# Kernel tuning notes

Hardware: AMD Instinct MI355X
Metric: run time of the kernel (lower is better)

The kernel has to match this reference:

```python
import jax, jax.numpy as jnp
import numpy as np

DIM = 1024
HEADS = 16
HD = DIM // HEADS          # 64
HID = 4 * DIM              # 4096
TPF = 1374                 # tokens_per_frame
LR = 0.1
NS_ITERS = 5
TTT_STEPS = 2
B, S = 2, 4
SN = S * TPF               # 5496


def _newton_schulz(G, iters=NS_ITERS):
    """Muon Newton-Schulz orthogonalization (quintic iteration)."""
    a, b, c = 3.4445, -4.7750, 2.0315
    X = G / (jnp.linalg.norm(G) + 1e-7)
    transposed = G.shape[0] > G.shape[1]
    if transposed:
        X = X.T
    for _ in range(iters):
        A = X @ X.T                      # [m,m], m = min(rows, cols)
        X = a * X + (b * A + c * (A @ A)) @ X
    return X.T if transposed else X


def _muon_update(p, g):
    return p - LR * _newton_schulz(g)


def setup_inputs() -> dict:
    key = jax.random.key(0)
    ks = jax.random.split(key, 8)
    inp = {
        "x": jax.random.normal(ks[0], (B, SN, DIM), jnp.float32),
        "qkv_w": jax.random.normal(ks[1], (DIM, 3 * DIM), jnp.float32) * (DIM ** -0.5),
        "qkv_b": jnp.zeros((3 * DIM,), jnp.float32),
        "qn_scale": jnp.ones((HD,), jnp.float32),
        "qn_bias": jnp.zeros((HD,), jnp.float32),
        "kn_scale": jnp.ones((HD,), jnp.float32),
        "kn_bias": jnp.zeros((HD,), jnp.float32),
        # theta: lecun-normal scale (std = 1/sqrt(fan_in))
        "ttt_gate": jax.random.normal(ks[2], (DIM, HID), jnp.float32) * (DIM ** -0.5),
        "ttt_val": jax.random.normal(ks[3], (DIM, HID), jnp.float32) * (DIM ** -0.5),
        "ttt_proj": jax.random.normal(ks[4], (HID, DIM), jnp.float32) * (HID ** -0.5),
        "proj_w": jax.random.normal(ks[5], (DIM, DIM), jnp.float32) * (DIM ** -0.5),
        "proj_b": jnp.zeros((DIM,), jnp.float32),
    }
    return inp


def reference(x, qkv_w, qkv_b, qn_scale, qn_bias, kn_scale, kn_bias,
              ttt_gate, ttt_val, ttt_proj, proj_w, proj_b):
    Bx, SNx, _ = x.shape
    qkv = x @ qkv_w + qkv_b                       # [B, SN, 3*DIM]
    q, k, v = jnp.split(qkv, 3, axis=-1)
    q = q.reshape(Bx, SNx, HEADS, HD)
    k = k.reshape(Bx, SNx, HEADS, HD)
    # per-head L2 normalize then affine NormLayer (x*scale + bias)
    q = q / (jnp.linalg.norm(q, axis=-1, keepdims=True) + 1e-6) * qn_scale + qn_bias
    k = k / (jnp.linalg.norm(k, axis=-1, keepdims=True) + 1e-6) * kn_scale + kn_bias
    q_ttt = q.reshape(-1, DIM)                    # [B*SN, DIM]
    k_ttt = k.reshape(-1, DIM)
    # no short_conv param at init -> v_mixed is identity, so v_target == v
    v_ttt = v.reshape(-1, DIM)

    theta = {"gate": ttt_gate, "val": ttt_val, "proj": ttt_proj}

    def loss_fn(p):
        h = jax.nn.swish(k_ttt @ p["gate"]) * (k_ttt @ p["val"])   # [B*SN, HID]
        pred = h @ p["proj"]                                        # [B*SN, DIM]
        return jnp.mean((pred - v_ttt) ** 2)

    for _ in range(TTT_STEPS):
        grads = jax.grad(loss_fn)(theta)
        theta = {kk: _muon_update(theta[kk], grads[kk]) for kk in theta}

    h_q = jax.nn.swish(q_ttt @ theta["gate"]) * (q_ttt @ theta["val"])
    o = (h_q @ theta["proj"]) @ proj_w + proj_b
    return o.reshape(Bx, SNx, DIM)
```

## Files before the change

### kernel.cpp

```cpp
#include <hip/hip_runtime.h>
#include <stdint.h>

#define NTOK 10992
#define NTOKA 11264
#define FCHK 5632
#define PMi 4194304

typedef unsigned short u16;
typedef __attribute__((ext_vector_type(8))) __bf16 b8;
typedef __attribute__((ext_vector_type(4))) float f32x4;

__device__ __forceinline__ u16 f2b(float f) {
  union { float f; uint32_t u; } v; v.f = f;
  return (u16)((v.u + 0x7fffu + ((v.u >> 16) & 1u)) >> 16);
}
__device__ __forceinline__ float b2f(u16 b) {
  union { uint32_t u; float f; } v; v.u = ((uint32_t)b) << 16; return v.f;
}
__device__ __forceinline__ uint2 pk4(u16 a, u16 b, u16 c, u16 d) {
  uint2 r; r.x = (uint32_t)a | ((uint32_t)b << 16); r.y = (uint32_t)c | ((uint32_t)d << 16);
  return r;
}
__device__ __forceinline__ void gload16(const u16* g, u16* l) {
  __builtin_amdgcn_global_load_lds((const __attribute__((address_space(1))) void*)(const void*)g,
                                   (__attribute__((address_space(3))) void*)(void*)l, 16, 0, 0);
}

struct GA {
  const u16* A[3]; const u16* B[3];
  void* C[3]; u16* O1[3]; u16* OT[3];
  const void* E0[3]; const u16* E1[3];
  int lda[3], ldb[3];
  int M, N, K, ldc, ldo1, ldt, lde0, lde1;
  float p0, p1;
};

template <int EPI, int SPLIT>
__global__ __launch_bounds__(256, 2) void gemm_bt(GA g) {
  __shared__ u16 As[128 * 32];
  __shared__ u16 Bs[128 * 32];
  int bz = blockIdx.z, koff = 0, klen = g.K;
  if constexpr (SPLIT) { koff = (bz & 1) * (g.K >> 1); bz >>= 1; klen = g.K >> 1; }
  const u16* __restrict__ A = g.A[bz] + koff;
  const u16* __restrict__ B = g.B[bz] + koff;
  const int lda = g.lda[bz], ldb = g.ldb[bz];
  const int m0 = blockIdx.y * 128, n0 = blockIdx.x * 128;
  const int tid = threadIdx.x, w = tid >> 6, lane = tid & 63;
  const int wr = (w >> 1) * 64, wc = (w & 1) * 64;
  const int ln = lane & 15, lq = lane >> 4;

  f32x4 acc[4][4];
#pragma unroll
  for (int i = 0; i < 4; ++i)
#pragma unroll
    for (int j = 0; j < 4; ++j)
#pragma unroll
      for (int r = 0; r < 4; ++r) acc[i][j][r] = 0.f;

  const u16* Ag = A + (size_t)(m0 + 32 * w + (lane >> 2)) * lda + (lane & 3) * 8;
  const u16* Bg = B + (size_t)(n0 + 32 * w + (lane >> 2)) * ldb + (lane & 3) * 8;
  u16* AsW = &As[w * 1024];
  u16* BsW = &Bs[w * 1024];
  const int nkt = klen >> 5;

  for (int kt = 0; kt < nkt; ++kt) {
    __syncthreads();
    gload16(Ag, AsW);
    gload16(Ag + (size_t)16 * lda, AsW + 512);
    gload16(Bg, BsW);
    gload16(Bg + (size_t)16 * ldb, BsW + 512);
    Ag += 32; Bg += 32;
    __syncthreads();
    b8 af[4], bfr[4];
#pragma unroll
    for (int i = 0; i < 4; ++i) af[i] = *(const b8*)&As[(wr + i * 16 + ln) * 32 + lq * 8];
#pragma unroll
    for (int j = 0; j < 4; ++j) bfr[j] = *(const b8*)&Bs[(wc + j * 16 + ln) * 32 + lq * 8];
#pragma unroll
    for (int i = 0; i < 4; ++i)
#pragma unroll
      for (int j = 0; j < 4; ++j)
        acc[i][j] = __builtin_amdgcn_mfma_f32_16x16x32_bf16(af[i], bfr[j], acc[i][j], 0, 0, 0);
  }

  float* Cf = (float*)g.C[bz];
  u16* Cb = (u16*)g.C[bz];
  u16* O1 = g.O1[bz];
  u16* OT = g.OT[bz];
  const float* E0f = (const float*)g.E0[bz];
  const u16* E0b = (const u16*)g.E0[bz];
  const u16* E1b = g.E1[bz];

#pragma unroll
  for (int i = 0; i < 4; ++i) {
    const int mb = m0 + wr + i * 16 + lq * 4;
    if (mb >= g.M) continue;
#pragma unroll
    for (int j = 0; j < 4; ++j) {
      const int n = n0 + wc + j * 16 + ln;
      if (n >= g.N) continue;
      float vv[4];
#pragma unroll
      for (int r = 0; r < 4; ++r) vv[r] = acc[i][j][r];
      if constexpr (EPI == 0) {
#pragma unroll
        for (int r = 0; r < 4; ++r) Cb[(size_t)(mb + r) * g.ldc + n] = f2b(vv[r]);
      } else if constexpr (EPI == 1) {
        const float bias = E0f[n];
#pragma unroll
        for (int r = 0; r < 4; ++r) Cb[(size_t)(mb + r) * g.ldc + n] = f2b(vv[r] + bias);
      } else if constexpr (EPI == 3) {
        u16 oq[4];
#pragma unroll
        for (int r = 0; r < 4; ++r) {
          const int m = mb + r;
          Cb[(size_t)m * g.ldc + n] = f2b(vv[r]);
          const float zg = b2f(E0b[(size_t)m * g.lde0 + n]);
          const float s = 1.f / (1.f + __expf(-zg));
          const u16 ub = f2b(zg * s * vv[r]);
          O1[(size_t)m * g.ldo1 + n] = ub;
          oq[r] = ub;
        }
        *(uint2*)&OT[(size_t)n * g.ldt + mb] = pk4(oq[0], oq[1], oq[2], oq[3]);
      } else if constexpr (EPI == 4) {
#pragma unroll
        for (int r = 0; r < 4; ++r) {
          const int m = mb + r;
          const float zg = b2f(E0b[(size_t)m * g.lde0 + n]);
          const float s = 1.f / (1.f + __expf(-zg));
          Cb[(size_t)m * g.ldc + n] = f2b(zg * s * vv[r]);
        }
      } else if constexpr (EPI == 5) {
        u16 cq[4], oq[4];
#pragma unroll
        for (int r = 0; r < 4; ++r) {
          const int m = mb + r;
          const float zg = b2f(E0b[(size_t)m * g.lde0 + n]);
          const float zv = b2f(E1b[(size_t)m * g.lde1 + n]);
          const float s = 1.f / (1.f + __expf(-zg));
          cq[r] = f2b(vv[r] * zv * s * (1.f + zg * (1.f - s)));
          oq[r] = f2b(vv[r] * zg * s);
        }
        *(uint2*)&Cb[(size_t)n * g.ldt + mb] = pk4(cq[0], cq[1], cq[2], cq[3]);
        *(uint2*)&O1[(size_t)n * g.ldt + mb] = pk4(oq[0], oq[1], oq[2], oq[3]);
      } else if constexpr (EPI == 6) {
        const float bias = E0f[n];
#pragma unroll
        for (int r = 0; r < 4; ++r) Cf[(size_t)(mb + r) * g.ldc + n] = vv[r] + bias;
      } else if constexpr (EPI == 8) {
#pragma unroll
        for (int r = 0; r < 4; ++r) atomicAdd(&Cf[(size_t)(mb + r) * g.ldc + n], vv[r]);
      } else if constexpr (EPI == 9) {
        u16 cq[4];
#pragma unroll
        for (int r = 0; r < 4; ++r) {
          const int m = mb + r;
          const u16 ub = f2b(g.p0 * b2f(E0b[(size_t)m * g.lde0 + n]) + vv[r]);
          Cb[(size_t)m * g.ldc + n] = ub;
          cq[r] = ub;
        }
        *(uint2*)&OT[(size_t)n * g.ldt + mb] = pk4(cq[0], cq[1], cq[2], cq[3]);
      }
    }
  }
}

template <int EPI>
__global__ __launch_bounds__(256, 2) void gemm64(GA g) {
  __shared__ u16 As[64 * 32];
  __shared__ u16 Bs[64 * 32];
  const int bz = blockIdx.z;
  const u16* __restrict__ A = g.A[bz];
  const u16* __restrict__ B = g.B[bz];
  const int lda = g.lda[bz], ldb = g.ldb[bz];
  const int m0 = blockIdx.y * 64, n0 = blockIdx.x * 64;
  const int tid = threadIdx.x, w = tid >> 6, lane = tid & 63;
  const int wr = (w >> 1) * 32, wc = (w & 1) * 32;
  const int ln = lane & 15, lq = lane >> 4;

  f32x4 acc[2][2];
#pragma unroll
  for (int i = 0; i < 2; ++i)
#pragma unroll
    for (int j = 0; j < 2; ++j)
#pragma unroll
      for (int r = 0; r < 4; ++r) acc[i][j][r] = 0.f;

  const u16* Ag = A + (size_t)(m0 + 16 * w + (lane >> 2)) * lda + (lane & 3) * 8;
  const u16* Bg = B + (size_t)(n0 + 16 * w + (lane >> 2)) * ldb + (lane & 3) * 8;
  u16* AsW = &As[w * 512];
  u16* BsW = &Bs[w * 512];
  const int nkt = g.K >> 5;

  for (int kt = 0; kt < nkt; ++kt) {
    __syncthreads();
    gload16(Ag, AsW);
    gload16(Bg, BsW);
    Ag += 32; Bg += 32;
    __syncthreads();
    b8 af[2], bfr[2];
#pragma unroll
    for (int i = 0; i < 2; ++i) af[i] = *(const b8*)&As[(wr + i * 16 + ln) * 32 + lq * 8];
#pragma unroll
    for (int j = 0; j < 2; ++j) bfr[j] = *(const b8*)&Bs[(wc + j * 16 + ln) * 32 + lq * 8];
#pragma unroll
    for (int i = 0; i < 2; ++i)
#pragma unroll
      for (int j = 0; j < 2; ++j)
        acc[i][j] = __builtin_amdgcn_mfma_f32_16x16x32_bf16(af[i], bfr[j], acc[i][j], 0, 0, 0);
  }

  float* Cf = (float*)g.C[bz];
  u16* Cb = (u16*)g.C[bz];
  u16* OT = g.OT[bz];
  const float* E0f = (const float*)g.E0[bz];
  const u16* E0b = (const u16*)g.E0[bz];

#pragma unroll
  for (int i = 0; i < 2; ++i) {
    const int mb = m0 + wr + i * 16 + lq * 4;
    if (mb >= g.M) continue;
#pragma unroll
    for (int j = 0; j < 2; ++j) {
      const int n = n0 + wc + j * 16 + ln;
      if (n >= g.N) continue;
      float vv[4];
#pragma unroll
      for (int r = 0; r < 4; ++r) vv[r] = acc[i][j][r];
      if constexpr (EPI == 0) {
#pragma unroll
        for (int r = 0; r < 4; ++r) Cb[(size_t)(mb + r) * g.ldc + n] = f2b(vv[r]);
      } else if constexpr (EPI == 2) {
        u16 cq[4];
#pragma unroll
        for (int r = 0; r < 4; ++r) {
          const int m = mb + r;
          const u16 ub = f2b((vv[r] - b2f(E0b[(size_t)m * g.lde0 + n])) * g.p0);
          Cb[(size_t)m * g.ldc + n] = ub;
          cq[r] = ub;
        }
        *(uint2*)&OT[(size_t)n * g.ldt + mb] = pk4(cq[0], cq[1], cq[2], cq[3]);
      } else if constexpr (EPI == 6) {
        const float bias = E0f[n];
#pragma unroll
        for (int r = 0; r < 4; ++r) Cf[(size_t)(mb + r) * g.ldc + n] = vv[r] + bias;
      } else if constexpr (EPI == 7) {
#pragma unroll
        for (int r = 0; r < 4; ++r) {
          const int m = mb + r;
          Cb[(size_t)m * g.ldc + n] =
              f2b(g.p0 * b2f(E0b[(size_t)m * g.lde0 + n]) + g.p1 * vv[r]);
        }
      }
    }
  }
}

__global__ __launch_bounds__(256) void norm_qkv(const u16* __restrict__ qkvB,
    const float* __restrict__ qs, const float* __restrict__ qbi,
    const float* __restrict__ ks, const float* __restrict__ kbi,
    u16* __restrict__ qb, u16* __restrict__ kb, u16* __restrict__ vb) {
  const int tok = blockIdx.x;
  const int t = threadIdx.x;
  const int d = t * 4;
  const u16* row = qkvB + (size_t)tok * 3072;
  const uint2 qu = *(const uint2*)(row + d);
  const uint2 ku = *(const uint2*)(row + 1024 + d);
  *(uint2*)(vb + (size_t)tok * 1024 + d) = *(const uint2*)(row + 2048 + d);
  float q0 = b2f(qu.x & 0xffff), q1 = b2f(qu.x >> 16), q2 = b2f(qu.y & 0xffff), q3 = b2f(qu.y >> 16);
  float k0 = b2f(ku.x & 0xffff), k1 = b2f(ku.x >> 16), k2 = b2f(ku.y & 0xffff), k3 = b2f(ku.y >> 16);
  float sq = q0 * q0 + q1 * q1 + q2 * q2 + q3 * q3;
  float sk = k0 * k0 + k1 * k1 + k2 * k2 + k3 * k3;
  for (int off = 1; off < 16; off <<= 1) { sq += __shfl_xor(sq, off); sk += __shfl_xor(sk, off); }
  const float rq = 1.f / (sqrtf(sq) + 1e-6f);
  const float rk = 1.f / (sqrtf(sk) + 1e-6f);
  const int hd = d & 63;
  const float4 qsv = *(const float4*)(qs + hd);
  const float4 qbv = *(const float4*)(qbi + hd);
  const float4 ksv = *(const float4*)(ks + hd);
  const float4 kbv = *(const float4*)(kbi + hd);
  uint64_t pq = (uint64_t)f2b(q0 * rq * qsv.x + qbv.x)
              | ((uint64_t)f2b(q1 * rq * qsv.y + qbv.y) << 16)
              | ((uint64_t)f2b(q2 * rq * qsv.z + qbv.z) << 32)
              | ((uint64_t)f2b(q3 * rq * qsv.w + qbv.w) << 48);
  uint64_t pk = (uint64_t)f2b(k0 * rk * ksv.x + kbv.x)
              | ((uint64_t)f2b(k1 * rk * ksv.y + kbv.y) << 16)
              | ((uint64_t)f2b(k2 * rk * ksv.z + kbv.z) << 32)
              | ((uint64_t)f2b(k3 * rk * ksv.w + kbv.w) << 48);
  *(uint64_t*)(qb + (size_t)tok * 1024 + d) = pq;
  *(uint64_t*)(kb + (size_t)tok * 1024 + d) = pk;
}

__global__ __launch_bounds__(256) void tr_b16(const u16* __restrict__ in, u16* __restrict__ out,
                                              int Cin, int Rtot, int Rval,
                                              size_t inStr, size_t outStr) {
  const int b = blockIdx.z;
  in += (size_t)b * inStr; out += (size_t)b * outStr;
  __shared__ u16 t[32][33];
  const int c0 = blockIdx.x * 32, r0 = blockIdx.y * 32;
  const int tx = threadIdx.x, ty = threadIdx.y;
#pragma unroll
  for (int yy = 0; yy < 4; ++yy) {
    const int rr = ty * 4 + yy;
    const int r = r0 + rr;
    t[rr][tx] = (r < Rval) ? in[(size_t)r * Cin + c0 + tx] : (u16)0;
  }
  __syncthreads();
#pragma unroll
  for (int yy = 0; yy < 4; ++yy) {
    const int cc = ty * 4 + yy;
    out[(size_t)(c0 + cc) * Rtot + r0 + tx] = t[tx][cc];
  }
}

__global__ __launch_bounds__(256) void tr_f32b(const float* __restrict__ in, u16* __restrict__ out,
                                               int Cin, int Rtot) {
  __shared__ u16 t[32][33];
  const int c0 = blockIdx.x * 32, r0 = blockIdx.y * 32;
  const int tx = threadIdx.x, ty = threadIdx.y;
#pragma unroll
  for (int yy = 0; yy < 4; ++yy) {
    const int rr = ty * 4 + yy;
    t[rr][tx] = f2b(in[(size_t)(r0 + rr) * Cin + c0 + tx]);
  }
  __syncthreads();
#pragma unroll
  for (int yy = 0; yy < 4; ++yy) {
    const int cc = ty * 4 + yy;
    out[(size_t)(c0 + cc) * Rtot + r0 + tx] = t[tx][cc];
  }
}

__global__ void cvt_k(const float* __restrict__ in, u16* __restrict__ out, int n) {
  const int i = blockIdx.x * 256 + threadIdx.x;
  if (i < n) out[i] = f2b(in[i]);
}

__global__ void diag_k(float* __restrict__ out, int n, float val) {
  const int i = blockIdx.x * 256 + threadIdx.x;
  if (i < n) out[i] = val;
}

__global__ __launch_bounds__(256) void sumsq_k(const float* __restrict__ g, float* __restrict__ out) {
  const int b = blockIdx.y;
  const float* p = g + (size_t)b * PMi;
  float s = 0.f;
  for (int i = blockIdx.x * 256 + threadIdx.x; i < PMi; i += gridDim.x * 256) {
    float v = p[i]; s += v * v;
  }
  for (int off = 32; off > 0; off >>= 1) s += __shfl_xor(s, off);
  __shared__ float red[4];
  if ((threadIdx.x & 63) == 0) red[threadIdx.x >> 6] = s;
  __syncthreads();
  if (threadIdx.x == 0) atomicAdd(out + b, red[0] + red[1] + red[2] + red[3]);
}

__global__ __launch_bounds__(256) void scale_k(const float* __restrict__ g, const float* __restrict__ ss,
                                               u16* __restrict__ Xb) {
  const int b = blockIdx.y;
  const float r = 1.f / (sqrtf(ss[b]) + 1e-7f);
  const size_t o = (size_t)b * PMi;
  for (int i = blockIdx.x * 256 + threadIdx.x; i < PMi; i += gridDim.x * 256)
    Xb[o + i] = f2b(g[o + i] * r);
}

__global__ __launch_bounds__(256) void muon_apply(const u16* __restrict__ Xb_,
    u16* __restrict__ Gt, u16* __restrict__ Vt, u16* __restrict__ Pt, u16* __restrict__ Pb) {
  const int b = blockIdx.z;
  __shared__ float xs[32][33];
  __shared__ u16 ns[32][33];
  const int j0 = blockIdx.x * 32;
  const int i0 = blockIdx.y * 32;
  const u16* X = Xb_ + (size_t)b * PMi;
  const int tx = threadIdx.x, ty = threadIdx.y;
#pragma unroll
  for (int yy = 0; yy < 4; ++yy) {
    const int r = ty * 4 + yy;
    xs[r][tx] = b2f(X[(size_t)(i0 + r) * 4096 + j0 + tx]);
  }
  __syncthreads();
  if (b < 2) {
    u16* T = b ? Vt : Gt;
#pragma unroll
    for (int yy = 0; yy < 4; ++yy) {
      const int rr = ty * 4 + yy;
      const size_t idx = (size_t)(j0 + rr) * 1024 + i0 + tx;
      T[idx] = f2b(b2f(T[idx]) - 0.1f * xs[tx][rr]);
    }
  } else {
#pragma unroll
    for (int yy = 0; yy < 4; ++yy) {
      const int rr = ty * 4 + yy;
      const size_t idx = (size_t)(j0 + rr) * 1024 + i0 + tx;
      const float nv = b2f(Pb[idx]) - 0.1f * xs[tx][rr];
      const u16 nb = f2b(nv);
      Pb[idx] = nb;
      ns[rr][tx] = nb;
    }
    __syncthreads();
#pragma unroll
    for (int yy = 0; yy < 4; ++yy) {
      const int rr = ty * 4 + yy;
      Pt[(size_t)(i0 + rr) * 4096 + j0 + tx] = ns[tx][rr];
    }
  }
}

static GA mk(const u16* A, const u16* B, void* C, int M, int N, int K,
             int lda, int ldb, int ldc) {
  GA a{};
  a.A[0] = a.A[1] = a.A[2] = A;
  a.B[0] = a.B[1] = a.B[2] = B;
  a.C[0] = a.C[1] = a.C[2] = C;
  a.lda[0] = a.lda[1] = a.lda[2] = lda;
  a.ldb[0] = a.ldb[1] = a.ldb[2] = ldb;
  a.M = M; a.N = N; a.K = K; a.ldc = ldc;
  return a;
}

extern "C" void kernel_launch(void* const* d_in, const int* in_sizes, int n_in,
                              void* d_out, int out_size, void* d_ws, size_t ws_size,
                              hipStream_t stream) {
  (void)in_sizes; (void)n_in;
  const float* x      = (const float*)d_in[0];
  const float* qkv_w  = (const float*)d_in[1];
  const float* qkv_b  = (const float*)d_in[2];
  const float* qn_s   = (const float*)d_in[3];
  const float* qn_b   = (const float*)d_in[4];
  const float* kn_s   = (const float*)d_in[5];
  const float* kn_b   = (const float*)d_in[6];
  const float* g_gate = (const float*)d_in[7];
  const float* g_val  = (const float*)d_in[8];
  const float* g_proj = (const float*)d_in[9];
  const float* proj_w = (const float*)d_in[10];
  const float* proj_b = (const float*)d_in[11];
  float* out = (float*)d_out;

  const size_t PM = PMi;
  const size_t TD = (size_t)NTOKA * 1024;

  const size_t NEED1 = 253231360 + 4096;
  const size_t NEED2 = 127926528 + 177209344 + 4096;
  if (ws_size < NEED1) {
    diag_k<<<dim3((out_size + 255) / 256), dim3(256), 0, stream>>>(out, out_size,
                                                                   (float)(ws_size >> 20));
    return;
  }
  const int CHKr = (ws_size >= NEED2) ? 2816 : 1408;

  char* p = (char*)d_ws;
  auto carve = [&](size_t bytes) { char* r = p; p += (bytes + 255) & ~(size_t)255; return (void*)r; };
  auto cdiv = [](int a, int b) { return (a + b - 1) / b; };

  u16* Gt     = (u16*)carve(PM * 2);
  u16* Vt     = (u16*)carve(PM * 2);
  u16* Pt     = (u16*)carve(PM * 2);
  u16* Pb     = (u16*)carve(PM * 2);
  u16* projWt = (u16*)carve(1048576ull * 2);
  u16* qb     = (u16*)carve(TD * 2);
  u16* kb     = (u16*)carve(TD * 2);
  u16* vT     = (u16*)carve(TD * 2);
  u16* kT     = (u16*)carve(TD * 2);
  float* ssq  = (float*)carve(256);
  char* arena = p;

  u16* xb     = (u16*)arena;
  u16* qkvWt  = (u16*)(arena + 23068672);
  u16* qkvB   = (u16*)(arena + 29360128);
  u16* vb_tmp = (u16*)(arena + 96894976);
  const size_t CB = (size_t)CHKr * 4096 * 2;
  const size_t DP = (size_t)CHKr * 1024 * 2;
  u16* zg     = (u16*)arena;
  u16* zv     = (u16*)(arena + CB);
  u16* hh     = (u16*)(arena + 2 * CB);
  u16* hT     = (u16*)(arena + 3 * CB);
  u16* dzvT   = (u16*)(arena + 4 * CB);
  u16* dpredT = (u16*)(arena + 5 * CB);
  u16* dpredb = (u16*)(arena + 5 * CB + DP);
  float* gAll = (float*)(arena + 5 * CB + 2 * DP);
  u16* XAb  = (u16*)arena;
  u16* XAbT = (u16*)(arena + 25165824);
  u16* XBb  = (u16*)(arena + 50331648);
  u16* XBbT = (u16*)(arena + 75497472);
  u16* Ab   = (u16*)(arena + 100663296);
  u16* Wb   = (u16*)(arena + 106954752);
  u16* zgc = (u16*)arena;
  u16* oc  = (u16*)(arena + 46137344);

  const dim3 blk(256), tb32(32, 8);
  const float inv2 = 2.0f / (10992.0f * 1024.0f);
  const float nsa = 3.4445f, nsb = -4.7750f, nsc = 2.0315f;

  cvt_k<<<dim3(43968), blk, 0, stream>>>(x, xb, NTOK * 1024);
  cvt_k<<<dim3(16384), blk, 0, stream>>>(g_proj, Pb, (int)PM);
  tr_f32b<<<dim3(96, 32), tb32, 0, stream>>>(qkv_w, qkvWt, 3072, 1024);
  tr_f32b<<<dim3(32, 32), tb32, 0, stream>>>(proj_w, projWt, 1024, 1024);
  tr_f32b<<<dim3(128, 32), tb32, 0, stream>>>(g_gate, Gt, 4096, 1024);
  tr_f32b<<<dim3(128, 32), tb32, 0, stream>>>(g_val, Vt, 4096, 1024);
  tr_f32b<<<dim3(32, 128), tb32, 0, stream>>>(g_proj, Pt, 1024, 4096);

  {
    GA a = mk(xb, qkvWt, qkvB, NTOK, 3072, 1024, 1024, 1024, 3072);
    a.E0[0] = a.E0[1] = a.E0[2] = qkv_b;
    gemm_bt<1, 0><<<dim3(24, 86, 1), blk, 0, stream>>>(a);
  }
  norm_qkv<<<dim3(NTOK), blk, 0, stream>>>(qkvB, qn_s, qn_b, kn_s, kn_b, qb, kb, vb_tmp);
  tr_b16<<<dim3(32, 352, 1), tb32, 0, stream>>>(kb, kT, 1024, NTOKA, NTOK, 0, 0);
  tr_b16<<<dim3(32, 352, 1), tb32, 0, stream>>>(vb_tmp, vT, 1024, NTOKA, NTOK, 0, 0);

  for (int step = 0; step < 2; ++step) {
    hipMemsetAsync(gAll, 0, 3 * PM * 4, stream);
    for (int c0 = 0; c0 < NTOK; c0 += CHKr) {
      const int vc = (NTOK - c0 < CHKr) ? (NTOK - c0) : CHKr;
      const int mt = cdiv(vc, 128);
      const u16* kc = kb + (size_t)c0 * 1024;
      if (vc < CHKr)
        hipMemsetAsync(hT, 0, 2 * CB + DP, stream);
      gemm_bt<0, 0><<<dim3(32, mt, 1), blk, 0, stream>>>(
          mk(kc, Gt, zg, vc, 4096, 1024, 1024, 1024, 4096));
      {
        GA a = mk(kc, Vt, zv, vc, 4096, 1024, 1024, 1024, 4096);
        a.O1[0] = hh; a.ldo1 = 4096; a.OT[0] = hT; a.ldt = CHKr;
        a.E0[0] = zg; a.lde0 = 4096;
        gemm_bt<3, 0><<<dim3(32, mt, 1), blk, 0, stream>>>(a);
      }
      {
        GA a = mk(Pt, hh, dpredT, 1024, vc, 4096, 4096, 4096, CHKr);
        a.OT[0] = dpredb; a.ldt = 1024;
        a.E0[0] = vT + c0; a.lde0 = NTOKA; a.p0 = inv2;
        gemm64<2><<<dim3(cdiv(vc, 64), 16, 1), blk, 0, stream>>>(a);
      }
      if (vc < CHKr)
        hipMemsetAsync(hh, 0, CB, stream);
      {
        GA a = mk(dpredb, Pb, hh, vc, 4096, 1024, 1024, 1024, 0);
        a.O1[0] = dzvT; a.ldt = CHKr;
        a.E0[0] = zg; a.lde0 = 4096; a.E1[0] = zv; a.lde1 = 4096;
        gemm_bt<5, 0><<<dim3(32, mt, 1), blk, 0, stream>>>(a);
      }
      {
        GA a{};
        a.A[0] = kT + c0; a.A[1] = kT + c0; a.A[2] = dpredT;
        a.lda[0] = NTOKA; a.lda[1] = NTOKA; a.lda[2] = CHKr;
        a.B[0] = hh; a.B[1] = dzvT; a.B[2] = hT;
        a.ldb[0] = a.ldb[1] = a.ldb[2] = CHKr;
        a.C[0] = gAll; a.C[1] = gAll + PM; a.C[2] = gAll + 2 * PM;
        a.M = 1024; a.N = 4096; a.K = CHKr; a.ldc = 4096;
        gemm_bt<8, 1><<<dim3(32, 8, 6), blk, 0, stream>>>(a);
      }
    }
    hipMemsetAsync(ssq, 0, 16, stream);
    sumsq_k<<<dim3(512, 3), blk, 0, stream>>>(gAll, ssq);
    scale_k<<<dim3(2048, 3), blk, 0, stream>>>(gAll, ssq, XAb);
    tr_b16<<<dim3(128, 32, 3), tb32, 0, stream>>>(XAb, XAbT, 4096, 1024, 1024, PM, PM);

    u16* Xi_b = XAb; u16* Xi_bT = XAbT;
    u16* Xo_b = XBb; u16* Xo_bT = XBbT;
    for (int it = 0; it < 5; ++it) {
      {
        GA a{};
        for (int b = 0; b < 3; ++b) {
          a.A[b] = Xi_b + (size_t)b * PM; a.B[b] = Xi_b + (size_t)b * PM;
          a.C[b] = Ab + (size_t)b * 1048576;
          a.lda[b] = 4096; a.ldb[b] = 4096;
        }
        a.M = 1024; a.N = 1024; a.K = 4096; a.ldc = 1024;
        gemm64<0><<<dim3(16, 16, 3), blk, 0, stream>>>(a);
      }
      {
        GA a{};
        for (int b = 0; b < 3; ++b) {
          a.A[b] = Ab + (size_t)b * 1048576; a.B[b] = Ab + (size_t)b * 1048576;
          a.C[b] = Wb + (size_t)b * 1048576; a.E0[b] = Ab + (size_t)b * 1048576;
          a.lda[b] = 1024; a.ldb[b] = 1024;
        }
        a.M = 1024; a.N = 1024; a.K = 1024; a.ldc = 1024; a.lde0 = 1024;
        a.p0 = nsb; a.p1 = nsc;
        gemm64<7><<<dim3(16, 16, 3), blk, 0, stream>>>(a);
      }
      {
        GA a{};
        for (int b = 0; b < 3; ++b) {
          a.A[b] = Wb + (size_t)b * 1048576; a.B[b] = Xi_bT + (size_t)b * PM;
          a.C[b] = Xo_b + (size_t)b * PM; a.OT[b] = Xo_bT + (size_t)b * PM;
          a.E0[b] = Xi_b + (size_t)b * PM;
          a.lda[b] = 1024; a.ldb[b] = 1024;
        }
        a.M = 1024; a.N = 4096; a.K = 1024; a.ldc = 4096; a.ldt = 1024;
        a.lde0 = 4096; a.p0 = nsa;
        gemm_bt<9, 0><<<dim3(32, 8, 3), blk, 0, stream>>>(a);
      }
      u16* tb = Xi_b; Xi_b = Xo_b; Xo_b = tb;
      u16* tt = Xi_bT; Xi_bT = Xo_bT; Xo_bT = tt;
    }
    muon_apply<<<dim3(128, 32, 3), tb32, 0, stream>>>(Xi_b, Gt, Vt, Pt, Pb);
  }

  for (int fc = 0; fc < 2; ++fc) {
    const int c0 = fc * FCHK;
    const int vc = (NTOK - c0 < FCHK) ? (NTOK - c0) : FCHK;
    const int mt = cdiv(vc, 128), mt64 = cdiv(vc, 64);
    const u16* qc = qb + (size_t)c0 * 1024;
    gemm_bt<0, 0><<<dim3(32, mt, 1), blk, 0, stream>>>(
        mk(qc, Gt, zgc, vc, 4096, 1024, 1024, 1024, 4096));
    {
      GA a = mk(qc, Vt, zgc, vc, 4096, 1024, 1024, 1024, 4096);
      a.E0[0] = zgc; a.lde0 = 4096;
      gemm_bt<4, 0><<<dim3(32, mt, 1), blk, 0, stream>>>(a);
    }
    gemm64<0><<<dim3(16, mt64, 1), blk, 0, stream>>>(
        mk(zgc, Pt, oc, vc, 1024, 4096, 4096, 4096, 1024));
    {
      GA a = mk(oc, projWt, out + (size_t)c0 * 1024, vc, 1024, 1024, 1024, 1024, 1024);
      a.E0[0] = proj_b;
      gemm64<6><<<dim3(16, mt64, 1), blk, 0, stream>>>(a);
    }
  }
}
```

Measured before the change: 6.681 ms.

## Exploit symmetry in Newton-Schulz Gram GEMMs and vectorize transposed-MFMA epilogues

```diff
diff --git a/kernel.cpp b/kernel.cpp
--- a/kernel.cpp
+++ b/kernel.cpp
@@ -20,6 +20,10 @@
 __device__ __forceinline__ uint2 pk4(u16 a, u16 b, u16 c, u16 d) {
   uint2 r; r.x = (uint32_t)a | ((uint32_t)b << 16); r.y = (uint32_t)c | ((uint32_t)d << 16);
   return r;
+}
+__device__ __forceinline__ void up4(uint2 u, float* f) {
+  f[0] = b2f((u16)(u.x & 0xffff)); f[1] = b2f((u16)(u.x >> 16));
+  f[2] = b2f((u16)(u.y & 0xffff)); f[3] = b2f((u16)(u.y >> 16));
 }
 __device__ __forceinline__ void gload16(const u16* g, u16* l) {
   __builtin_amdgcn_global_load_lds((const __attribute__((address_space(1))) void*)(const void*)g,
@@ -79,8 +83,12 @@
 #pragma unroll
     for (int i = 0; i < 4; ++i)
 #pragma unroll
-      for (int j = 0; j < 4; ++j)
-        acc[i][j] = __builtin_amdgcn_mfma_f32_16x16x32_bf16(af[i], bfr[j], acc[i][j], 0, 0, 0);
+      for (int j = 0; j < 4; ++j) {
+        if constexpr (EPI == 5)
+          acc[i][j] = __builtin_amdgcn_mfma_f32_16x16x32_bf16(af[i], bfr[j], acc[i][j], 0, 0, 0);
+        else
+          acc[i][j] = __builtin_amdgcn_mfma_f32_16x16x32_bf16(bfr[j], af[i], acc[i][j], 0, 0, 0);
+      }
   }
 
   float* Cf = (float*)g.C[bz];
@@ -91,46 +99,15 @@
   const u16* E0b = (const u16*)g.E0[bz];
   const u16* E1b = g.E1[bz];
 
-#pragma unroll
-  for (int i = 0; i < 4; ++i) {
-    const int mb = m0 + wr + i * 16 + lq * 4;
-    if (mb >= g.M) continue;
-#pragma unroll
-    for (int j = 0; j < 4; ++j) {
-      const int n = n0 + wc + j * 16 + ln;
-      if (n >= g.N) continue;
-      float vv[4];
-#pragma unroll
-      for (int r = 0; r < 4; ++r) vv[r] = acc[i][j][r];
-      if constexpr (EPI == 0) {
-#pragma unroll
-        for (int r = 0; r < 4; ++r) Cb[(size_t)(mb + r) * g.ldc + n] = f2b(vv[r]);
-      } else if constexpr (EPI == 1) {
-        const float bias = E0f[n];
-#pragma unroll
-        for (int r = 0; r < 4; ++r) Cb[(size_t)(mb + r) * g.ldc + n] = f2b(vv[r] + bias);
-      } else if constexpr (EPI == 3) {
-        u16 oq[4];
-#pragma unroll
-        for (int r = 0; r < 4; ++r) {
-          const int m = mb + r;
-          Cb[(size_t)m * g.ldc + n] = f2b(vv[r]);
-          const float zg = b2f(E0b[(size_t)m * g.lde0 + n]);
-          const float s = 1.f / (1.f + __expf(-zg));
-          const u16 ub = f2b(zg * s * vv[r]);
-          O1[(size_t)m * g.ldo1 + n] = ub;
-          oq[r] = ub;
-        }
-        *(uint2*)&OT[(size_t)n * g.ldt + mb] = pk4(oq[0], oq[1], oq[2], oq[3]);
-      } else if constexpr (EPI == 4) {
-#pragma unroll
-        for (int r = 0; r < 4; ++r) {
-          const int m = mb + r;
-          const float zg = b2f(E0b[(size_t)m * g.lde0 + n]);
-          const float s = 1.f / (1.f + __expf(-zg));
-          Cb[(size_t)m * g.ldc + n] = f2b(zg * s * vv[r]);
-        }
-      } else if constexpr (EPI == 5) {
+  if constexpr (EPI == 5) {
+#pragma unroll
+    for (int i = 0; i < 4; ++i) {
+      const int mb = m0 + wr + i * 16 + lq * 4;
+      if (mb >= g.M) continue;
+#pragma unroll
+      for (int j = 0; j < 4; ++j) {
+        const int n = n0 + wc + j * 16 + ln;
+        if (n >= g.N) continue;
         u16 cq[4], oq[4];
 #pragma unroll
         for (int r = 0; r < 4; ++r) {
@@ -138,28 +115,71 @@
           const float zg = b2f(E0b[(size_t)m * g.lde0 + n]);
           const float zv = b2f(E1b[(size_t)m * g.lde1 + n]);
           const float s = 1.f / (1.f + __expf(-zg));
-          cq[r] = f2b(vv[r] * zv * s * (1.f + zg * (1.f - s)));
-          oq[r] = f2b(vv[r] * zg * s);
+          const float vv = acc[i][j][r];
+          cq[r] = f2b(vv * zv * s * (1.f + zg * (1.f - s)));
+          oq[r] = f2b(vv * zg * s);
         }
         *(uint2*)&Cb[(size_t)n * g.ldt + mb] = pk4(cq[0], cq[1], cq[2], cq[3]);
         *(uint2*)&O1[(size_t)n * g.ldt + mb] = pk4(oq[0], oq[1], oq[2], oq[3]);
-      } else if constexpr (EPI == 6) {
-        const float bias = E0f[n];
-#pragma unroll
-        for (int r = 0; r < 4; ++r) Cf[(size_t)(mb + r) * g.ldc + n] = vv[r] + bias;
-      } else if constexpr (EPI == 8) {
-#pragma unroll
-        for (int r = 0; r < 4; ++r) atomicAdd(&Cf[(size_t)(mb + r) * g.ldc + n], vv[r]);
-      } else if constexpr (EPI == 9) {
-        u16 cq[4];
-#pragma unroll
-        for (int r = 0; r < 4; ++r) {
-          const int m = mb + r;
-          const u16 ub = f2b(g.p0 * b2f(E0b[(size_t)m * g.lde0 + n]) + vv[r]);
-          Cb[(size_t)m * g.ldc + n] = ub;
-          cq[r] = ub;
+      }
+    }
+  } else {
+#pragma unroll
+    for (int i = 0; i < 4; ++i) {
+      const int m = m0 + wr + i * 16 + ln;
+      if (m >= g.M) continue;
+#pragma unroll
+      for (int j = 0; j < 4; ++j) {
+        const int nb = n0 + wc + j * 16 + lq * 4;
+        if (nb >= g.N) continue;
+        float vv[4];
+#pragma unroll
+        for (int r = 0; r < 4; ++r) vv[r] = acc[i][j][r];
+        if constexpr (EPI == 0) {
+          *(uint2*)&Cb[(size_t)m * g.ldc + nb] = pk4(f2b(vv[0]), f2b(vv[1]), f2b(vv[2]), f2b(vv[3]));
+        } else if constexpr (EPI == 1) {
+          const float4 bs = *(const float4*)(E0f + nb);
+          *(uint2*)&Cb[(size_t)m * g.ldc + nb] =
+              pk4(f2b(vv[0] + bs.x), f2b(vv[1] + bs.y), f2b(vv[2] + bs.z), f2b(vv[3] + bs.w));
+        } else if constexpr (EPI == 3) {
+          float z4[4]; up4(*(const uint2*)&E0b[(size_t)m * g.lde0 + nb], z4);
+          u16 cz[4], hb[4];
+#pragma unroll
+          for (int r = 0; r < 4; ++r) {
+            const float s = 1.f / (1.f + __expf(-z4[r]));
+            cz[r] = f2b(vv[r]);
+            hb[r] = f2b(z4[r] * s * vv[r]);
+          }
+          *(uint2*)&Cb[(size_t)m * g.ldc + nb] = pk4(cz[0], cz[1], cz[2], cz[3]);
+          *(uint2*)&O1[(size_t)m * g.ldo1 + nb] = pk4(hb[0], hb[1], hb[2], hb[3]);
+#pragma unroll
+          for (int r = 0; r < 4; ++r) OT[(size_t)(nb + r) * g.ldt + m] = hb[r];
+        } else if constexpr (EPI == 4) {
+          float z4[4]; up4(*(const uint2*)&E0b[(size_t)m * g.lde0 + nb], z4);
+          u16 ob[4];
+#pragma unroll
+          for (int r = 0; r < 4; ++r) {
+            const float s = 1.f / (1.f + __expf(-z4[r]));
+            ob[r] = f2b(z4[r] * s * vv[r]);
+          }
+          *(uint2*)&Cb[(size_t)m * g.ldc + nb] = pk4(ob[0], ob[1], ob[2], ob[3]);
+        } else if constexpr (EPI == 6) {
+          const float4 bs = *(const float4*)(E0f + nb);
+          float4 o; o.x = vv[0] + bs.x; o.y = vv[1] + bs.y; o.z = vv[2] + bs.z; o.w = vv[3] + bs.w;
+          *(float4*)&Cf[(size_t)m * g.ldc + nb] = o;
+        } else if constexpr (EPI == 8) {
+          float* dst = &Cf[(size_t)m * g.ldc + nb];
+#pragma unroll
+          for (int r = 0; r < 4; ++r) atomicAdd(dst + r, vv[r]);
+        } else if constexpr (EPI == 9) {
+          float x4[4]; up4(*(const uint2*)&E0b[(size_t)m * g.lde0 + nb], x4);
+          u16 cq[4];
+#pragma unroll
+          for (int r = 0; r < 4; ++r) cq[r] = f2b(g.p0 * x4[r] + vv[r]);
+          *(uint2*)&Cb[(size_t)m * g.ldc + nb] = pk4(cq[0], cq[1], cq[2], cq[3]);
+#pragma unroll
+          for (int r = 0; r < 4; ++r) OT[(size_t)(nb + r) * g.ldt + m] = cq[r];
         }
-        *(uint2*)&OT[(size_t)n * g.ldt + mb] = pk4(cq[0], cq[1], cq[2], cq[3]);
       }
     }
   }
@@ -167,6 +187,9 @@
 
 template <int EPI>
 __global__ __launch_bounds__(256, 2) void gemm64(GA g) {
+  if constexpr (EPI == 10 || EPI == 11) {
+    if (blockIdx.x > blockIdx.y) return;
+  }
   __shared__ u16 As[64 * 32];
   __shared__ u16 Bs[64 * 32];
   const int bz = blockIdx.z;
@@ -207,7 +230,7 @@
     for (int i = 0; i < 2; ++i)
 #pragma unroll
       for (int j = 0; j < 2; ++j)
-        acc[i][j] = __builtin_amdgcn_mfma_f32_16x16x32_bf16(af[i], bfr[j], acc[i][j], 0, 0, 0);
+        acc[i][j] = __builtin_amdgcn_mfma_f32_16x16x32_bf16(bfr[j], af[i], acc[i][j], 0, 0, 0);
   }
 
   float* Cf = (float*)g.C[bz];
@@ -215,41 +238,51 @@
   u16* OT = g.OT[bz];
   const float* E0f = (const float*)g.E0[bz];
   const u16* E0b = (const u16*)g.E0[bz];
+  const bool offdiag = (blockIdx.x != blockIdx.y);
 
 #pragma unroll
   for (int i = 0; i < 2; ++i) {
-    const int mb = m0 + wr + i * 16 + lq * 4;
-    if (mb >= g.M) continue;
+    const int m = m0 + wr + i * 16 + ln;
+    if (m >= g.M) continue;
 #pragma unroll
     for (int j = 0; j < 2; ++j) {
-      const int n = n0 + wc + j * 16 + ln;
-      if (n >= g.N) continue;
+      const int nb = n0 + wc + j * 16 + lq * 4;
+      if (nb >= g.N) continue;
       float vv[4];
 #pragma unroll
       for (int r = 0; r < 4; ++r) vv[r] = acc[i][j][r];
       if constexpr (EPI == 0) {
-#pragma unroll
-        for (int r = 0; r < 4; ++r) Cb[(size_t)(mb + r) * g.ldc + n] = f2b(vv[r]);
+        *(uint2*)&Cb[(size_t)m * g.ldc + nb] = pk4(f2b(vv[0]), f2b(vv[1]), f2b(vv[2]), f2b(vv[3]));
       } else if constexpr (EPI == 2) {
+        float e4[4]; up4(*(const uint2*)&E0b[(size_t)m * g.lde0 + nb], e4);
         u16 cq[4];
 #pragma unroll
-        for (int r = 0; r < 4; ++r) {
-          const int m = mb + r;
-          const u16 ub = f2b((vv[r] - b2f(E0b[(size_t)m * g.lde0 + n])) * g.p0);
-          Cb[(size_t)m * g.ldc + n] = ub;
-          cq[r] = ub;
+        for (int r = 0; r < 4; ++r) cq[r] = f2b((vv[r] - e4[r]) * g.p0);
+        *(uint2*)&Cb[(size_t)m * g.ldc + nb] = pk4(cq[0], cq[1], cq[2], cq[3]);
+#pragma unroll
+        for (int r = 0; r < 4; ++r) OT[(size_t)(nb + r) * g.ldt + m] = cq[r];
+      } else if constexpr (EPI == 6) {
+        const float4 bs = *(const float4*)(E0f + nb);
+        float4 o; o.x = vv[0] + bs.x; o.y = vv[1] + bs.y; o.z = vv[2] + bs.z; o.w = vv[3] + bs.w;
+        *(float4*)&Cf[(size_t)m * g.ldc + nb] = o;
+      } else if constexpr (EPI == 10) {
+        u16 cq[4];
+#pragma unroll
+        for (int r = 0; r < 4; ++r) cq[r] = f2b(vv[r]);
+        *(uint2*)&Cb[(size_t)m * g.ldc + nb] = pk4(cq[0], cq[1], cq[2], cq[3]);
+        if (offdiag) {
+#pragma unroll
+          for (int r = 0; r < 4; ++r) Cb[(size_t)(nb + r) * g.ldc + m] = cq[r];
         }
-        *(uint2*)&OT[(size_t)n * g.ldt + mb] = pk4(cq[0], cq[1], cq[2], cq[3]);
-      } else if constexpr (EPI == 6) {
-        const float bias = E0f[n];
-#pragma unroll
-        for (int r = 0; r < 4; ++r) Cf[(size_t)(mb + r) * g.ldc + n] = vv[r] + bias;
-      } else if constexpr (EPI == 7) {
-#pragma unroll
-        for (int r = 0; r < 4; ++r) {
-          const int m = mb + r;
-          Cb[(size_t)m * g.ldc + n] =
-              f2b(g.p0 * b2f(E0b[(size_t)m * g.lde0 + n]) + g.p1 * vv[r]);
+      } else if constexpr (EPI == 11) {
+        float e4[4]; up4(*(const uint2*)&E0b[(size_t)m * g.lde0 + nb], e4);
+        u16 cq[4];
+#pragma unroll
+        for (int r = 0; r < 4; ++r) cq[r] = f2b(g.p0 * e4[r] + g.p1 * vv[r]);
+        *(uint2*)&Cb[(size_t)m * g.ldc + nb] = pk4(cq[0], cq[1], cq[2], cq[3]);
+        if (offdiag) {
+#pragma unroll
+          for (int r = 0; r < 4; ++r) Cb[(size_t)(nb + r) * g.ldc + m] = cq[r];
         }
       }
     }
@@ -441,12 +474,13 @@
 
   const size_t NEED1 = 253231360 + 4096;
   const size_t NEED2 = 127926528 + 177209344 + 4096;
+  const size_t NEED3 = 127926528ull + 304087040ull + 4096;
   if (ws_size < NEED1) {
     diag_k<<<dim3((out_size + 255) / 256), dim3(256), 0, stream>>>(out, out_size,
                                                                    (float)(ws_size >> 20));
     return;
   }
-  const int CHKr = (ws_size >= NEED2) ? 2816 : 1408;
+  const int CHKr = (ws_size >= NEED3) ? 5632 : (ws_size >= NEED2) ? 2816 : 1408;
 
   char* p = (char*)d_ws;
   auto carve = [&](size_t bytes) { char* r = p; p += (bytes + 255) & ~(size_t)255; return (void*)r; };
@@ -565,7 +599,7 @@
           a.lda[b] = 4096; a.ldb[b] = 4096;
         }
         a.M = 1024; a.N = 1024; a.K = 4096; a.ldc = 1024;
-        gemm64<0><<<dim3(16, 16, 3), blk, 0, stream>>>(a);
+        gemm64<10><<<dim3(16, 16, 3), blk, 0, stream>>>(a);
       }
       {
         GA a{};
@@ -576,7 +610,7 @@
         }
         a.M = 1024; a.N = 1024; a.K = 1024; a.ldc = 1024; a.lde0 = 1024;
         a.p0 = nsb; a.p1 = nsc;
-        gemm64<7><<<dim3(16, 16, 3), blk, 0, stream>>>(a);
+        gemm64<11><<<dim3(16, 16, 3), blk, 0, stream>>>(a);
       }
       {
         GA a{};
```

Result: slower. 10.12 ms (+51.5%).

## Fuse gate/value GEMMs into one kernel and exploit symmetry in Newton-Schulz

Applied to the files above, without the earlier changes.

```diff
diff --git a/kernel.cpp b/kernel.cpp
--- a/kernel.cpp
+++ b/kernel.cpp
@@ -109,27 +109,6 @@
         const float bias = E0f[n];
 #pragma unroll
         for (int r = 0; r < 4; ++r) Cb[(size_t)(mb + r) * g.ldc + n] = f2b(vv[r] + bias);
-      } else if constexpr (EPI == 3) {
-        u16 oq[4];
-#pragma unroll
-        for (int r = 0; r < 4; ++r) {
-          const int m = mb + r;
-          Cb[(size_t)m * g.ldc + n] = f2b(vv[r]);
-          const float zg = b2f(E0b[(size_t)m * g.lde0 + n]);
-          const float s = 1.f / (1.f + __expf(-zg));
-          const u16 ub = f2b(zg * s * vv[r]);
-          O1[(size_t)m * g.ldo1 + n] = ub;
-          oq[r] = ub;
-        }
-        *(uint2*)&OT[(size_t)n * g.ldt + mb] = pk4(oq[0], oq[1], oq[2], oq[3]);
-      } else if constexpr (EPI == 4) {
-#pragma unroll
-        for (int r = 0; r < 4; ++r) {
-          const int m = mb + r;
-          const float zg = b2f(E0b[(size_t)m * g.lde0 + n]);
-          const float s = 1.f / (1.f + __expf(-zg));
-          Cb[(size_t)m * g.ldc + n] = f2b(zg * s * vv[r]);
-        }
       } else if constexpr (EPI == 5) {
         u16 cq[4], oq[4];
 #pragma unroll
@@ -143,10 +122,6 @@
         }
         *(uint2*)&Cb[(size_t)n * g.ldt + mb] = pk4(cq[0], cq[1], cq[2], cq[3]);
         *(uint2*)&O1[(size_t)n * g.ldt + mb] = pk4(oq[0], oq[1], oq[2], oq[3]);
-      } else if constexpr (EPI == 6) {
-        const float bias = E0f[n];
-#pragma unroll
-        for (int r = 0; r < 4; ++r) Cf[(size_t)(mb + r) * g.ldc + n] = vv[r] + bias;
       } else if constexpr (EPI == 8) {
 #pragma unroll
         for (int r = 0; r < 4; ++r) atomicAdd(&Cf[(size_t)(mb + r) * g.ldc + n], vv[r]);
@@ -166,7 +141,102 @@
 }
 
 template <int EPI>
+__global__ __launch_bounds__(256, 2) void gemm_gv(GA g) {
+  __shared__ u16 As[128 * 32];
+  __shared__ u16 Gs[128 * 32];
+  __shared__ u16 Vs[128 * 32];
+  const u16* __restrict__ A = g.A[0];
+  const u16* __restrict__ G = g.B[0];
+  const u16* __restrict__ V = g.B[1];
+  const int lda = g.lda[0], ldb = g.ldb[0];
+  const int m0 = blockIdx.y * 128, n0 = blockIdx.x * 128;
+  const int tid = threadIdx.x, w = tid >> 6, lane = tid & 63;
+  const int wr = (w >> 1) * 64, wc = (w & 1) * 64;
+  const int ln = lane & 15, lq = lane >> 4;
+
+  f32x4 ag[4][4], av[4][4];
+#pragma unroll
+  for (int i = 0; i < 4; ++i)
+#pragma unroll
+    for (int j = 0; j < 4; ++j)
+#pragma unroll
+      for (int r = 0; r < 4; ++r) { ag[i][j][r] = 0.f; av[i][j][r] = 0.f; }
+
+  const u16* Agp = A + (size_t)(m0 + 32 * w + (lane >> 2)) * lda + (lane & 3) * 8;
+  const u16* Ggp = G + (size_t)(n0 + 32 * w + (lane >> 2)) * ldb + (lane & 3) * 8;
+  const u16* Vgp = V + (size_t)(n0 + 32 * w + (lane >> 2)) * ldb + (lane & 3) * 8;
+  u16* AsW = &As[w * 1024];
+  u16* GsW = &Gs[w * 1024];
+  u16* VsW = &Vs[w * 1024];
+  const int nkt = g.K >> 5;
+
+  for (int kt = 0; kt < nkt; ++kt) {
+    __syncthreads();
+    gload16(Agp, AsW);
+    gload16(Agp + (size_t)16 * lda, AsW + 512);
+    gload16(Ggp, GsW);
+    gload16(Ggp + (size_t)16 * ldb, GsW + 512);
+    gload16(Vgp, VsW);
+    gload16(Vgp + (size_t)16 * ldb, VsW + 512);
+    Agp += 32; Ggp += 32; Vgp += 32;
+    __syncthreads();
+    b8 af[4], gf[4], vf[4];
+#pragma unroll
+    for (int i = 0; i < 4; ++i) af[i] = *(const b8*)&As[(wr + i * 16 + ln) * 32 + lq * 8];
+#pragma unroll
+    for (int j = 0; j < 4; ++j) gf[j] = *(const b8*)&Gs[(wc + j * 16 + ln) * 32 + lq * 8];
+#pragma unroll
+    for (int j = 0; j < 4; ++j) vf[j] = *(const b8*)&Vs[(wc + j * 16 + ln) * 32 + lq * 8];
+#pragma unroll
+    for (int i = 0; i < 4; ++i)
+#pragma unroll
+      for (int j = 0; j < 4; ++j) {
+        ag[i][j] = __builtin_amdgcn_mfma_f32_16x16x32_bf16(af[i], gf[j], ag[i][j], 0, 0, 0);
+        av[i][j] = __builtin_amdgcn_mfma_f32_16x16x32_bf16(af[i], vf[j], av[i][j], 0, 0, 0);
+      }
+  }
+
+  u16* Zg = (u16*)g.C[0];
+  u16* Zv = g.O1[0];
+  u16* Hh = g.O1[1];
+  u16* HT = g.OT[0];
+
+#pragma unroll
+  for (int i = 0; i < 4; ++i) {
+    const int mb = m0 + wr + i * 16 + lq * 4;
+    if (mb >= g.M) continue;
+#pragma unroll
+    for (int j = 0; j < 4; ++j) {
+      const int n = n0 + wc + j * 16 + ln;
+      if (n >= g.N) continue;
+      u16 hq[4];
+#pragma unroll
+      for (int r = 0; r < 4; ++r) {
+        const int m = mb + r;
+        const float zg = ag[i][j][r];
+        const float zv = av[i][j][r];
+        const float s = 1.f / (1.f + __expf(-zg));
+        const u16 hb = f2b(zg * s * zv);
+        if constexpr (EPI == 0) {
+          Zg[(size_t)m * g.ldc + n] = f2b(zg);
+          Zv[(size_t)m * g.ldc + n] = f2b(zv);
+          Hh[(size_t)m * g.ldc + n] = hb;
+          hq[r] = hb;
+        } else {
+          Zg[(size_t)m * g.ldc + n] = hb;
+        }
+      }
+      if constexpr (EPI == 0)
+        *(uint2*)&HT[(size_t)n * g.ldt + mb] = pk4(hq[0], hq[1], hq[2], hq[3]);
+    }
+  }
+}
+
+template <int EPI>
 __global__ __launch_bounds__(256, 2) void gemm64(GA g) {
+  if constexpr (EPI == 10 || EPI == 11) {
+    if (blockIdx.x > blockIdx.y) return;
+  }
   __shared__ u16 As[64 * 32];
   __shared__ u16 Bs[64 * 32];
   const int bz = blockIdx.z;
@@ -215,6 +285,7 @@
   u16* OT = g.OT[bz];
   const float* E0f = (const float*)g.E0[bz];
   const u16* E0b = (const u16*)g.E0[bz];
+  const bool offdiag = (blockIdx.x != blockIdx.y);
 
 #pragma unroll
   for (int i = 0; i < 2; ++i) {
@@ -244,13 +315,24 @@
         const float bias = E0f[n];
 #pragma unroll
         for (int r = 0; r < 4; ++r) Cf[(size_t)(mb + r) * g.ldc + n] = vv[r] + bias;
-      } else if constexpr (EPI == 7) {
+      } else if constexpr (EPI == 10) {
+        u16 cq[4];
 #pragma unroll
         for (int r = 0; r < 4; ++r) {
-          const int m = mb + r;
-          Cb[(size_t)m * g.ldc + n] =
-              f2b(g.p0 * b2f(E0b[(size_t)m * g.lde0 + n]) + g.p1 * vv[r]);
-        }
+          cq[r] = f2b(vv[r]);
+          Cb[(size_t)(mb + r) * g.ldc + n] = cq[r];
+        }
+        if (offdiag)
+          *(uint2*)&Cb[(size_t)n * g.ldc + mb] = pk4(cq[0], cq[1], cq[2], cq[3]);
+      } else if constexpr (EPI == 11) {
+        u16 cq[4];
+#pragma unroll
+        for (int r = 0; r < 4; ++r) {
+          cq[r] = f2b(g.p0 * b2f(E0b[(size_t)(mb + r) * g.lde0 + n]) + g.p1 * vv[r]);
+          Cb[(size_t)(mb + r) * g.ldc + n] = cq[r];
+        }
+        if (offdiag)
+          *(uint2*)&Cb[(size_t)n * g.ldc + mb] = pk4(cq[0], cq[1], cq[2], cq[3]);
       }
     }
   }
@@ -484,8 +566,10 @@
   u16* XBbT = (u16*)(arena + 75497472);
   u16* Ab   = (u16*)(arena + 100663296);
   u16* Wb   = (u16*)(arena + 106954752);
-  u16* zgc = (u16*)arena;
-  u16* oc  = (u16*)(arena + 46137344);
+  const int FCN  = (CHKr >= 2816) ? 1 : 2;
+  const int FBLK = (FCN == 1) ? NTOK : FCHK;
+  u16* hbuf = (u16*)arena;
+  u16* oc   = (u16*)(arena + ((FCN == 1) ? 92274688ull : 46137344ull));
 
   const dim3 blk(256), tb32(32, 8);
   const float inv2 = 2.0f / (10992.0f * 1024.0f);
@@ -516,13 +600,13 @@
       const u16* kc = kb + (size_t)c0 * 1024;
       if (vc < CHKr)
         hipMemsetAsync(hT, 0, 2 * CB + DP, stream);
-      gemm_bt<0, 0><<<dim3(32, mt, 1), blk, 0, stream>>>(
-          mk(kc, Gt, zg, vc, 4096, 1024, 1024, 1024, 4096));
       {
-        GA a = mk(kc, Vt, zv, vc, 4096, 1024, 1024, 1024, 4096);
-        a.O1[0] = hh; a.ldo1 = 4096; a.OT[0] = hT; a.ldt = CHKr;
-        a.E0[0] = zg; a.lde0 = 4096;
-        gemm_bt<3, 0><<<dim3(32, mt, 1), blk, 0, stream>>>(a);
+        GA a{};
+        a.A[0] = kc; a.lda[0] = 1024;
+        a.B[0] = Gt; a.B[1] = Vt; a.ldb[0] = 1024;
+        a.C[0] = zg; a.O1[0] = zv; a.O1[1] = hh; a.OT[0] = hT;
+        a.M = vc; a.N = 4096; a.K = 1024; a.ldc = 4096; a.ldt = CHKr;
+        gemm_gv<0><<<dim3(32, mt, 1), blk, 0, stream>>>(a);
       }
       {
         GA a = mk(Pt, hh, dpredT, 1024, vc, 4096, 4096, 4096, CHKr);
@@ -565,7 +649,7 @@
           a.lda[b] = 4096; a.ldb[b] = 4096;
         }
         a.M = 1024; a.N = 1024; a.K = 4096; a.ldc = 1024;
-        gemm64<0><<<dim3(16, 16, 3), blk, 0, stream>>>(a);
+        gemm64<10><<<dim3(16, 16, 3), blk, 0, stream>>>(a);
       }
       {
         GA a{};
@@ -576,7 +660,7 @@
         }
         a.M = 1024; a.N = 1024; a.K = 1024; a.ldc = 1024; a.lde0 = 1024;
         a.p0 = nsb; a.p1 = nsc;
-        gemm64<7><<<dim3(16, 16, 3), blk, 0, stream>>>(a);
+        gemm64<11><<<dim3(16, 16, 3), blk, 0, stream>>>(a);
       }
       {
         GA a{};
@@ -596,20 +680,21 @@
     muon_apply<<<dim3(128, 32, 3), tb32, 0, stream>>>(Xi_b, Gt, Vt, Pt, Pb);
   }
 
-  for (int fc = 0; fc < 2; ++fc) {
-    const int c0 = fc * FCHK;
-    const int vc = (NTOK - c0 < FCHK) ? (NTOK - c0) : FCHK;
+  for (int fc = 0; fc < FCN; ++fc) {
+    const int c0 = fc * FBLK;
+    const int vc = (NTOK - c0 < FBLK) ? (NTOK - c0) : FBLK;
     const int mt = cdiv(vc, 128), mt64 = cdiv(vc, 64);
     const u16* qc = qb + (size_t)c0 * 1024;
-    gemm_bt<0, 0><<<dim3(32, mt, 1), blk, 0, stream>>>(
-        mk(qc, Gt, zgc, vc, 4096, 1024, 1024, 1024, 4096));
     {
-      GA a = mk(qc, Vt, zgc, vc, 4096, 1024, 1024, 1024, 4096);
-      a.E0[0] = zgc; a.lde0 = 4096;
-      gemm_bt<4, 0><<<dim3(32, mt, 1), blk, 0, stream>>>(a);
+      GA a{};
+      a.A[0] = qc; a.lda[0] = 1024;
+      a.B[0] = Gt; a.B[1] = Vt; a.ldb[0] = 1024;
+      a.C[0] = hbuf;
+      a.M = vc; a.N = 4096; a.K = 1024; a.ldc = 4096;
+      gemm_gv<1><<<dim3(32, mt, 1), blk, 0, stream>>>(a);
     }
     gemm64<0><<<dim3(16, mt64, 1), blk, 0, stream>>>(
-        mk(zgc, Pt, oc, vc, 1024, 4096, 4096, 4096, 1024));
+        mk(hbuf, Pt, oc, vc, 1024, 4096, 4096, 4096, 1024));
     {
       GA a = mk(oc, projWt, out + (size_t)c0 * 1024, vc, 1024, 1024, 1024, 1024, 1024);
       a.E0[0] = proj_b;
```

Measured after the change: 6.333 ms. -5.2%, faster.
